# Kernel optimization log

Measured on AMD Instinct MI355X. Metric: run time of the kernel, lower is better.

The kernel has to match this reference:

```python
import jax, jax.numpy as jnp
import numpy as np

LMAX = 2; C = 64; H = 8; D = C // H
N_NODES = 10000; N_EDGES = 160000
M = (LMAX + 1) ** 2                      # 9 spherical components
RAD_IN = 64; RAD_HID = 64
WNUM = (LMAX + 1) * C                    # per-edge CP-TP weights: one per (l, channel)
L_OF_M = jnp.array([l for l in range(LMAX + 1) for _ in range(2 * l + 1)])
LN_EPS = 1e-5


def _lin(x, W, b=None):
    # Linear over channel (last) dim; bias applied ONLY to scalar (m=0) component
    y = jnp.einsum('nmc,cd->nmd', x, W)
    if b is not None:
        y = y.at[:, 0, :].add(b)
    return y


def _cp_tp(x, sh, w_lc):
    # CP tensor product with SH: channelwise product, per-(l, channel) radial weight
    # x: [E, M, C], sh: [E, M], w_lc: [E, LMAX+1, C]
    return x * sh[:, :, None] * w_lc[:, L_OF_M, :]


def _radial(s, W1, b1, g, b, W2, off):
    h = s @ W1 + b1
    mu = h.mean(-1, keepdims=True)
    var = h.var(-1, keepdims=True)
    h = (h - mu) / jnp.sqrt(var + LN_EPS) * g + b
    h = jax.nn.silu(h)
    return (h @ W2 + off).reshape(-1, LMAX + 1, C)


def _smooth_lrelu(x, a=0.2):
    return (1 + a) / 2 * x + (1 - a) / 2 * x * (2 * jax.nn.sigmoid(x) - 1)


def _gate(x):
    c = x.shape[-1] // 2
    v = x[..., :c]
    g = jax.nn.sigmoid(x[:, 0, c:])[:, None, :]
    return jnp.concatenate([jax.nn.silu(v[:, :1, :]), v[:, 1:, :] * g], axis=1)


def _seg_softmax(a, idx, n):
    # numerically stable softmax over edges grouped by destination node
    m = jax.ops.segment_max(a, idx, num_segments=n)
    e = jnp.exp(a - m[idx])
    s = jax.ops.segment_sum(e, idx, num_segments=n)
    return e / (s[idx] + 1e-16)


def setup_inputs():
    key = jax.random.key(0)
    ks = jax.random.split(key, 16)
    def w(k, shape, fan_in):
        return jax.random.normal(k, shape, jnp.float32) / np.sqrt(fan_in)
    bound = 1.0 / np.sqrt(RAD_HID)
    return {
        'node_input': jax.random.normal(ks[0], (N_NODES, M, C), jnp.float32),
        'edge_attr': jax.random.normal(ks[1], (N_EDGES, M), jnp.float32),
        'edge_scalars': jax.random.normal(ks[2], (N_EDGES, RAD_IN), jnp.float32),
        'W_src': w(ks[3], (C, C), C), 'b_src': jnp.zeros((C,), jnp.float32),
        'W_dst': w(ks[4], (C, C), C),
        'rad_W1': w(ks[5], (RAD_IN, RAD_HID), RAD_IN),
        'rad_b1': jnp.zeros((RAD_HID,), jnp.float32),
        'rad_ln_g': jnp.ones((RAD_HID,), jnp.float32),
        'rad_ln_b': jnp.zeros((RAD_HID,), jnp.float32),
        'rad_W2': w(ks[6], (RAD_HID, WNUM), RAD_HID),
        'rad_offset': jax.random.uniform(ks[7], (WNUM,), jnp.float32, -bound, bound),
        'W_alpha': w(ks[8], (C, C), C), 'b_alpha': jnp.zeros((C,), jnp.float32),
        'alpha_dot': w(ks[9], (H, D), D),
        'W_value': w(ks[10], (C, 2 * C), C), 'b_value': jnp.zeros((2 * C,), jnp.float32),
        'W_proj': w(ks[11], (C, C), C), 'b_proj': jnp.zeros((C,), jnp.float32),
        'edge_src': jax.random.randint(ks[12], (N_EDGES,), 0, N_NODES),
        'edge_dst': jax.random.randint(ks[13], (N_EDGES,), 0, N_NODES),
        'batch': jnp.zeros((N_NODES,), jnp.int32),
    }


def reference(node_input, edge_attr, edge_scalars, W_src, b_src, W_dst,
              rad_W1, rad_b1, rad_ln_g, rad_ln_b, rad_W2, rad_offset,
              W_alpha, b_alpha, alpha_dot, W_value, b_value, W_proj, b_proj,
              edge_src, edge_dst, batch):
    # gather: per-edge merged message [E, M, C]
    msg = _lin(node_input, W_src, b_src)[edge_src] + _lin(node_input, W_dst)[edge_dst]
    # per-edge radial weights for both tensor products [E, LMAX+1, C]
    w_lc = _radial(edge_scalars, rad_W1, rad_b1, rad_ln_g, rad_ln_b, rad_W2, rad_offset)
    msg = _cp_tp(msg, edge_attr, w_lc)
    # alpha path: scalar channel only
    alpha = _lin(msg, W_alpha, b_alpha)[:, 0, :].reshape(-1, H, D)
    alpha = _smooth_lrelu(alpha)[:, None]                 # [E, 1, H, D]
    alpha = jnp.einsum('bikd,kd->bik', alpha, alpha_dot)  # [E, 1, H]
    alpha = _seg_softmax(alpha, edge_dst, N_NODES)        # dropout disabled (eval)
    # value path
    value = _gate(_lin(msg, W_value, b_value))
    value = _cp_tp(value, edge_attr, w_lc)
    value = value.reshape(N_EDGES, M, H, D)
    # scatter-aggregate to destination nodes
    out = jax.ops.segment_sum(value * alpha[:, :, :, None], edge_dst, num_segments=N_NODES)
    return _lin(out.reshape(N_NODES, M, C), W_proj, b_proj)
```

## Files before the change

kernel.cpp:

```cpp
#include <hip/hip_runtime.h>
#include <stdint.h>

#define NN 10000
#define NE 160000

struct BF16 { unsigned short v; };
typedef _Float16 h2_t __attribute__((ext_vector_type(2)));
typedef _Float16 f16x8 __attribute__((ext_vector_type(8)));
typedef float f32x4 __attribute__((ext_vector_type(4)));

__device__ __forceinline__ float cvt(float x) { return x; }
__device__ __forceinline__ float cvt(BF16 x) {
    union { unsigned int i; float f; } u; u.i = ((unsigned int)x.v) << 16; return u.f;
}
__device__ __forceinline__ unsigned short f2b_us(float f) {
    union { float f; unsigned int i; } v; v.f = f;
    unsigned int x = v.i;
    unsigned int lsb = (x >> 16) & 1u;
    x += 0x7fffu + lsb;
    return (unsigned short)(x >> 16);
}
__device__ __forceinline__ float rlane(float v, int l) {
    return __uint_as_float((unsigned int)__builtin_amdgcn_readlane(__float_as_uint(v), l));
}
__device__ __forceinline__ h2_t rlane_pk(h2_t v, int l) {
    union { h2_t h; unsigned int u; } c; c.h = v;
    c.u = (unsigned int)__builtin_amdgcn_readlane(c.u, l);
    return c.h;
}
__device__ __forceinline__ h2_t pkh2(float a, float b) {
    h2_t r; r[0] = (_Float16)a; r[1] = (_Float16)b; return r;
}
__device__ __forceinline__ float fdot2f(h2_t a, h2_t b, float c) {
#if __has_builtin(__builtin_amdgcn_fdot2)
    return __builtin_amdgcn_fdot2(a, b, c, false);
#else
    return fmaf((float)a[0], (float)b[0], fmaf((float)a[1], (float)b[1], c));
#endif
}
__device__ __forceinline__ float sigm(float x) { return 1.0f / (1.0f + __expf(-x)); }
__device__ __forceinline__ int clampi(int v, int hi) { return (unsigned)v >= (unsigned)hi ? 0 : v; }

__device__ __forceinline__ void stOut(float* p, size_t i, float v) { p[i] = v; }
__device__ __forceinline__ void stOut(unsigned short* p, size_t i, float v) { p[i] = f2b_us(v); }

__device__ __forceinline__ unsigned okey(float f) {
    unsigned b = __float_as_uint(f);
    return (b & 0x80000000u) ? ~b : (b | 0x80000000u);
}
__device__ __forceinline__ float okdec(unsigned k) {
    unsigned b = (k & 0x80000000u) ? (k ^ 0x80000000u) : ~k;
    return __uint_as_float(b);
}

__device__ __forceinline__ f16x8 ld8f16(const BF16* p) {
    uint4 v = *(const uint4*)p;
    unsigned w0 = v.x, w1 = v.y, w2 = v.z, w3 = v.w;
    f16x8 r;
    union { unsigned u; float f; } c;
    c.u = (w0 & 0xFFFFu) << 16;  r[0] = (_Float16)c.f;
    c.u = (w0 & 0xFFFF0000u);    r[1] = (_Float16)c.f;
    c.u = (w1 & 0xFFFFu) << 16;  r[2] = (_Float16)c.f;
    c.u = (w1 & 0xFFFF0000u);    r[3] = (_Float16)c.f;
    c.u = (w2 & 0xFFFFu) << 16;  r[4] = (_Float16)c.f;
    c.u = (w2 & 0xFFFF0000u);    r[5] = (_Float16)c.f;
    c.u = (w3 & 0xFFFFu) << 16;  r[6] = (_Float16)c.f;
    c.u = (w3 & 0xFFFF0000u);    r[7] = (_Float16)c.f;
    return r;
}
__device__ __forceinline__ f16x8 ld8f16(const float* p) {
    float4 a = *(const float4*)p;
    float4 b = *(const float4*)(p + 4);
    f16x8 r;
    r[0] = (_Float16)a.x; r[1] = (_Float16)a.y; r[2] = (_Float16)a.z; r[3] = (_Float16)a.w;
    r[4] = (_Float16)b.x; r[5] = (_Float16)b.y; r[6] = (_Float16)b.z; r[7] = (_Float16)b.w;
    return r;
}

__global__ void k0_zero(int* __restrict__ cnt, int* __restrict__ csr, int* __restrict__ flag,
                        float* __restrict__ nsum, unsigned* __restrict__ mseg,
                        float* __restrict__ sseg) {
    int i = blockIdx.x * blockDim.x + threadIdx.x;
    if (i == 0) *flag = 1;
    if (i < NN) cnt[i] = 0;
    if (i < NE) csr[i] = 0;
    if (i < NN * 8) { mseg[i] = 0u; sseg[i] = 0.f; }
    for (int j = i; j < NN * 576; j += gridDim.x * blockDim.x) nsum[j] = 0.f;
}

__global__ void kprobe(const unsigned short* __restrict__ x, int* __restrict__ flag) {
    int bad = 0;
    for (int i = threadIdx.x; i < 16384; i += blockDim.x) {
        unsigned e = (x[i] >> 7) & 0xFFu;
        bad += (e == 0xFFu);
    }
    if (bad > 0) atomicExch(flag, 0);
}

template<typename T>
__device__ void k1_body(const T* x, const T* Ws, const T* bs, const T* Wd,
                        _Float16* fs, _Float16* fd)
{
    int lane = threadIdx.x & 63;
    int wv = threadIdx.x >> 6;
    float ws[64], wd[64];
#pragma unroll
    for (int i = 0; i < 64; i++) { ws[i] = cvt(Ws[i * 64 + lane]); wd[i] = cvt(Wd[i * 64 + lane]); }
    float bsl = cvt(bs[lane]);
    const int ROWS = NN * 9;
    for (int r = blockIdx.x * 4 + wv; r < ROWS; r += gridDim.x * 4) {
        float xv = cvt(x[(size_t)r * 64 + lane]);
        float a0 = 0, a1 = 0, a2 = 0, a3 = 0, d0 = 0, d1 = 0, d2 = 0, d3 = 0;
#pragma unroll
        for (int i = 0; i < 64; i += 4) {
            float x0 = rlane(xv, i), x1 = rlane(xv, i + 1), x2 = rlane(xv, i + 2), x3 = rlane(xv, i + 3);
            a0 = fmaf(x0, ws[i], a0);     a1 = fmaf(x1, ws[i + 1], a1);
            a2 = fmaf(x2, ws[i + 2], a2); a3 = fmaf(x3, ws[i + 3], a3);
            d0 = fmaf(x0, wd[i], d0);     d1 = fmaf(x1, wd[i + 1], d1);
            d2 = fmaf(x2, wd[i + 2], d2); d3 = fmaf(x3, wd[i + 3], d3);
        }
        float as = a0 + a1 + a2 + a3;
        if ((r % 9) == 0) as += bsl;
        fs[(size_t)r * 64 + lane] = (_Float16)as;
        fd[(size_t)r * 64 + lane] = (_Float16)(d0 + d1 + d2 + d3);
    }
}

__global__ __launch_bounds__(256) void k1_feats(
    const void* x, const void* Ws, const void* bs, const void* Wd,
    _Float16* fs, _Float16* fd, const int* flag)
{
    if (*flag) k1_body((const BF16*)x, (const BF16*)Ws, (const BF16*)bs, (const BF16*)Wd, fs, fd);
    else       k1_body((const float*)x, (const float*)Ws, (const float*)bs, (const float*)Wd, fs, fd);
}

__global__ void k2a_count(const int* __restrict__ dst, int* __restrict__ cnt) {
    for (int e = blockIdx.x * blockDim.x + threadIdx.x; e < NE; e += gridDim.x * blockDim.x)
        atomicAdd(&cnt[clampi(dst[e], NN)], 1);
}

__global__ __launch_bounds__(1024) void k2b_scan(const int* __restrict__ cnt,
                                                 int* __restrict__ off, int* __restrict__ cur) {
    __shared__ int part[1024];
    int t = threadIdx.x;
    int base = t * 10;
    int loc[10]; int s = 0;
#pragma unroll
    for (int k = 0; k < 10; k++) { int i = base + k; int v = (i < NN) ? cnt[i] : 0; loc[k] = v; s += v; }
    part[t] = s; __syncthreads();
    for (int o = 1; o < 1024; o <<= 1) {
        int v = (t >= o) ? part[t - o] : 0;
        __syncthreads();
        part[t] += v;
        __syncthreads();
    }
    int run = (t == 0) ? 0 : part[t - 1];
#pragma unroll
    for (int k = 0; k < 10; k++) {
        int i = base + k;
        if (i < NN) { off[i] = run; cur[i] = run; run += loc[k]; }
    }
    if (t == 1023) off[NN] = part[1023];
}

__global__ void k2c_fill(const int* __restrict__ dst, int* __restrict__ cur, int* __restrict__ csr) {
    for (int e = blockIdx.x * blockDim.x + threadIdx.x; e < NE; e += gridDim.x * blockDim.x) {
        int d = clampi(dst[e], NN);
        int p = atomicAdd(&cur[d], 1);
        if ((unsigned)p < (unsigned)NE) csr[p] = e;
    }
}

template<typename T>
__device__ void k3m_body(const T* es, const T* W1, const T* b1g, const T* gg, const T* bbv,
                         const T* W2, const T* roff, _Float16* wlc,
                         _Float16 (*Yt)[200])
{
    const int lane = threadIdx.x & 63;
    const int c16 = lane & 15;
    const int kg  = lane >> 4;

    f16x8 bW1[4][2], bW2[12][2];
#pragma unroll
    for (int t = 0; t < 4; t++)
#pragma unroll
        for (int kh = 0; kh < 2; kh++) {
            f16x8 f;
#pragma unroll
            for (int j = 0; j < 8; j++) {
                int k = kh * 32 + kg * 8 + j;
                f[j] = (_Float16)cvt(W1[(size_t)k * 64 + t * 16 + c16]);
            }
            bW1[t][kh] = f;
        }
#pragma unroll
    for (int t = 0; t < 12; t++)
#pragma unroll
        for (int kh = 0; kh < 2; kh++) {
            f16x8 f;
#pragma unroll
            for (int j = 0; j < 8; j++) {
                int k = kh * 32 + kg * 8 + j;
                f[j] = (_Float16)cvt(W2[(size_t)k * 192 + t * 16 + c16]);
            }
            bW2[t][kh] = f;
        }
    float b1v[4], gv[4], bv[4], rv[12];
#pragma unroll
    for (int t = 0; t < 4; t++) {
        b1v[t] = cvt(b1g[t * 16 + c16]);
        gv[t]  = cvt(gg[t * 16 + c16]);
        bv[t]  = cvt(bbv[t * 16 + c16]);
    }
#pragma unroll
    for (int t = 0; t < 12; t++) rv[t] = cvt(roff[t * 16 + c16]);

    const int NT = NE / 16;
    for (int tile = blockIdx.x * 4 + (threadIdx.x >> 6); tile < NT; tile += gridDim.x * 4) {
        const int e0 = tile * 16;
        f16x8 a0 = ld8f16(&es[(size_t)(e0 + c16) * 64 + kg * 8]);
        f16x8 a1 = ld8f16(&es[(size_t)(e0 + c16) * 64 + 32 + kg * 8]);
        f32x4 h[4] = {{0,0,0,0},{0,0,0,0},{0,0,0,0},{0,0,0,0}};
#pragma unroll
        for (int t = 0; t < 4; t++) {
            h[t] = __builtin_amdgcn_mfma_f32_16x16x32_f16(a0, bW1[t][0], h[t], 0, 0, 0);
            h[t] = __builtin_amdgcn_mfma_f32_16x16x32_f16(a1, bW1[t][1], h[t], 0, 0, 0);
        }
#pragma unroll
        for (int r = 0; r < 4; r++) {
            float x0 = h[0][r] + b1v[0], x1 = h[1][r] + b1v[1];
            float x2 = h[2][r] + b1v[2], x3 = h[3][r] + b1v[3];
            float s = x0 + x1 + x2 + x3;
            float q = x0 * x0 + x1 * x1 + x2 * x2 + x3 * x3;
            s += __shfl_xor(s, 1, 64); q += __shfl_xor(q, 1, 64);
            s += __shfl_xor(s, 2, 64); q += __shfl_xor(q, 2, 64);
            s += __shfl_xor(s, 4, 64); q += __shfl_xor(q, 4, 64);
            s += __shfl_xor(s, 8, 64); q += __shfl_xor(q, 8, 64);
            float mu = s * (1.0f / 64.0f);
            float var = fmaxf(q * (1.0f / 64.0f) - mu * mu, 0.0f);
            float rs = rsqrtf(var + 1e-5f);
            int row = kg * 4 + r;
#pragma unroll
            for (int t = 0; t < 4; t++) {
                float xt = (t == 0) ? x0 : (t == 1) ? x1 : (t == 2) ? x2 : x3;
                float v = (xt - mu) * rs * gv[t] + bv[t];
                v = v * sigm(v);
                Yt[row][t * 16 + c16] = (_Float16)v;
            }
        }
        f16x8 a20 = *(const f16x8*)&Yt[c16][kg * 8];
        f16x8 a21 = *(const f16x8*)&Yt[c16][32 + kg * 8];
        f32x4 y[12] = {{0,0,0,0},{0,0,0,0},{0,0,0,0},{0,0,0,0},{0,0,0,0},{0,0,0,0},
                       {0,0,0,0},{0,0,0,0},{0,0,0,0},{0,0,0,0},{0,0,0,0},{0,0,0,0}};
#pragma unroll
        for (int t = 0; t < 12; t++) {
            y[t] = __builtin_amdgcn_mfma_f32_16x16x32_f16(a20, bW2[t][0], y[t], 0, 0, 0);
            y[t] = __builtin_amdgcn_mfma_f32_16x16x32_f16(a21, bW2[t][1], y[t], 0, 0, 0);
        }
#pragma unroll
        for (int t = 0; t < 12; t++)
#pragma unroll
            for (int r = 0; r < 4; r++)
                Yt[kg * 4 + r][t * 16 + c16] = (_Float16)(y[t][r] + rv[t]);
#pragma unroll
        for (int j = 0; j < 6; j++) {
            int c = lane + 64 * j;
            int row = c / 24;
            int cc = (c % 24) * 8;
            *(f16x8*)&wlc[(size_t)(e0 + row) * 192 + cc] = *(const f16x8*)&Yt[row][cc];
        }
    }
}

__global__ __launch_bounds__(256) void k3m_wlc(
    const void* es, const void* W1, const void* b1, const void* g, const void* bln,
    const void* W2, const void* roff, _Float16* wlc, const int* flag)
{
    __shared__ _Float16 Y[4][16][200];
    const int wv = threadIdx.x >> 6;
    if (*flag) k3m_body<BF16>((const BF16*)es, (const BF16*)W1, (const BF16*)b1, (const BF16*)g,
                              (const BF16*)bln, (const BF16*)W2, (const BF16*)roff, wlc, Y[wv]);
    else       k3m_body<float>((const float*)es, (const float*)W1, (const float*)b1, (const float*)g,
                               (const float*)bln, (const float*)W2, (const float*)roff, wlc, Y[wv]);
}

template<typename T>
__device__ void k4_body(const T* ea, const _Float16* fs, const _Float16* fd,
                        const _Float16* wlc, const T* Wa, const T* ba, const T* adot,
                        const int* esrc, const int* edst, float* alpha, unsigned* mseg)
{
    int lane = threadIdx.x & 63;
    int wv = threadIdx.x >> 6;
    int j2 = (lane & 31) * 2;
    h2_t wap[32];
#pragma unroll
    for (int i = 0; i < 32; i++)
        wap[i] = pkh2(cvt(Wa[(2 * i) * 64 + lane]), cvt(Wa[(2 * i + 1) * 64 + lane]));
    float bal = cvt(ba[lane]), adl = cvt(adot[lane]);
    for (int e = blockIdx.x * 4 + wv; e < NE; e += gridDim.x * 4) {
        int sn = clampi(esrc[e], NN), dn = clampi(edst[e], NN);
        h2_t fsp = *(const h2_t*)&fs[(size_t)sn * 576 + j2];
        h2_t fdp = *(const h2_t*)&fd[(size_t)dn * 576 + j2];
        h2_t wlp = *(const h2_t*)&wlc[(size_t)e * 192 + j2];
        float ea0 = cvt(ea[(size_t)e * 9]);
        float m0a = ((float)fsp[0] + (float)fdp[0]) * ea0 * (float)wlp[0];
        float m0b = ((float)fsp[1] + (float)fdp[1]) * ea0 * (float)wlp[1];
        h2_t m0p = pkh2(m0a, m0b);
        float a0 = bal, a1 = 0, a2 = 0, a3 = 0;
#pragma unroll
        for (int i = 0; i < 32; i += 4) {
            a0 = fdot2f(rlane_pk(m0p, i),     wap[i],     a0);
            a1 = fdot2f(rlane_pk(m0p, i + 1), wap[i + 1], a1);
            a2 = fdot2f(rlane_pk(m0p, i + 2), wap[i + 2], a2);
            a3 = fdot2f(rlane_pk(m0p, i + 3), wap[i + 3], a3);
        }
        float aw = a0 + a1 + a2 + a3;
        float f = aw * (0.2f + 0.8f * sigm(aw));
        float p = f * adl;
        p += __shfl_xor(p, 1, 64);
        p += __shfl_xor(p, 2, 64);
        p += __shfl_xor(p, 4, 64);
        if ((lane & 7) == 0) {
            alpha[(size_t)e * 8 + (lane >> 3)] = p;
            atomicMax(&mseg[dn * 8 + (lane >> 3)], okey(p));
        }
    }
}

__global__ __launch_bounds__(256) void k4_alpha(
    const void* ea, const _Float16* fs, const _Float16* fd, const _Float16* wlc,
    const void* Wa, const void* ba, const void* adot,
    const int* esrc, const int* edst, float* alpha, unsigned* mseg, const int* flag)
{
    if (*flag) k4_body((const BF16*)ea, fs, fd, wlc, (const BF16*)Wa, (const BF16*)ba,
                       (const BF16*)adot, esrc, edst, alpha, mseg);
    else       k4_body((const float*)ea, fs, fd, wlc, (const float*)Wa, (const float*)ba,
                       (const float*)adot, esrc, edst, alpha, mseg);
}

__global__ void k5b_expsum(const int* __restrict__ edst, const unsigned* __restrict__ mseg,
                           float* __restrict__ alpha, float* __restrict__ sseg) {
    int t = blockIdx.x * blockDim.x + threadIdx.x;
    if (t >= NE * 8) return;
    int e = t >> 3, h = t & 7;
    int dn = clampi(edst[e], NN);
    float m = okdec(mseg[dn * 8 + h]);
    float ex = __expf(alpha[t] - m);
    alpha[t] = ex;
    unsafeAtomicAdd(&sseg[dn * 8 + h], ex);
}

template<typename T>
__device__ void k6m_body(const int* off, const int* csr, const int* esrc,
                         const T* ea, const _Float16* fs, const _Float16* fd,
                         const _Float16* wlc, const T* Wv, const T* bv,
                         const float* alpha, const float* sseg, float* nsum,
                         _Float16 (*wlS)[16][72], float (*mtS)[20])
{
    const int lane = threadIdx.x & 63;
    const int wvid = threadIdx.x >> 6;
    const int c16 = lane & 15;
    const int kg  = lane >> 4;

    for (int gw = blockIdx.x * 4 + wvid; gw < NN * 2; gw += gridDim.x * 4) {
        const int n = gw >> 1;
        const int half = gw & 1;
        const int b = off[n], e_end = off[n + 1];
        if (b >= e_end) continue;

        f16x8 bfV[2][2], bfG[2][2];
        float bvv[2], bgv[2];
        int colg[2], hh[2];
        float invs[2];
#pragma unroll
        for (int t = 0; t < 2; t++) {
            colg[t] = (half * 2 + t) * 16 + c16;
            hh[t] = colg[t] >> 3;
            invs[t] = 1.0f / (sseg[n * 8 + hh[t]] + 1e-16f);
#pragma unroll
            for (int kh = 0; kh < 2; kh++) {
                f16x8 b8v, b8g;
#pragma unroll
                for (int j = 0; j < 8; j++) {
                    int k = kh * 32 + kg * 8 + j;
                    b8v[j] = (_Float16)cvt(Wv[(size_t)k * 128 + colg[t]]);
                    b8g[j] = (_Float16)cvt(Wv[(size_t)k * 128 + 64 + colg[t]]);
                }
                bfV[t][kh] = b8v; bfG[t][kh] = b8g;
            }
            bvv[t] = cvt(bv[colg[t]]);
            bgv[t] = cvt(bv[64 + colg[t]]);
        }

        const size_t fdb = (size_t)n * 576;
        const size_t nbase = (size_t)n * 576;

        for (int p0 = b; p0 < e_end; p0 += 16) {
            int pA = p0 + c16; if (pA >= e_end) pA = e_end - 1;
            const int eA = clampi(csr[pA], NE);
            const int snA = clampi(esrc[eA], NN);
            const size_t fsb = (size_t)snA * 576;
            const size_t wlb = (size_t)eA * 192;

#pragma unroll
            for (int l = 0; l < 3; l++)
#pragma unroll
                for (int kh = 0; kh < 2; kh++)
                    *(f16x8*)&wlS[l][c16][kh * 32 + kg * 8] =
                        *(const f16x8*)&wlc[wlb + (size_t)l * 64 + kh * 32 + kg * 8];
            float eao[9];
#pragma unroll
            for (int m = 0; m < 9; m++) eao[m] = cvt(ea[(size_t)eA * 9 + m]);
            if (kg == 0) {
#pragma unroll
                for (int m = 0; m < 9; m++) mtS[c16][m] = eao[m];
            }
            mtS[c16][10 + kg * 2]     = alpha[(size_t)eA * 8 + kg * 2];
            mtS[c16][10 + kg * 2 + 1] = alpha[(size_t)eA * 8 + kg * 2 + 1];

            float awm[2][4];
#pragma unroll
            for (int r = 0; r < 4; r++) {
                int row = kg * 4 + r;
                float vm = (p0 + row < e_end) ? 1.f : 0.f;
#pragma unroll
                for (int t = 0; t < 2; t++)
                    awm[t][r] = mtS[row][10 + hh[t]] * invs[t] * vm;
            }

            float gtv[2][4];
            {
                f16x8 a0, a1;
                {
                    f16x8 w0 = *(const f16x8*)&wlS[0][c16][kg * 8];
                    f16x8 w1 = *(const f16x8*)&wlS[0][c16][32 + kg * 8];
                    f16x8 fd0 = *(const f16x8*)&fd[fdb + kg * 8];
                    f16x8 fd1 = *(const f16x8*)&fd[fdb + 32 + kg * 8];
                    f16x8 fs0 = *(const f16x8*)&fs[fsb + kg * 8];
                    f16x8 fs1 = *(const f16x8*)&fs[fsb + 32 + kg * 8];
                    _Float16 eh = (_Float16)eao[0];
                    f16x8 ev;
#pragma unroll
                    for (int j = 0; j < 8; j++) ev[j] = eh;
                    a0 = (fs0 + fd0) * ev * w0;
                    a1 = (fs1 + fd1) * ev * w1;
                }
                f32x4 d[2] = {{0,0,0,0},{0,0,0,0}};
                f32x4 g[2] = {{0,0,0,0},{0,0,0,0}};
#pragma unroll
                for (int t = 0; t < 2; t++) {
                    d[t] = __builtin_amdgcn_mfma_f32_16x16x32_f16(a0, bfV[t][0], d[t], 0, 0, 0);
                    d[t] = __builtin_amdgcn_mfma_f32_16x16x32_f16(a1, bfV[t][1], d[t], 0, 0, 0);
                    g[t] = __builtin_amdgcn_mfma_f32_16x16x32_f16(a0, bfG[t][0], g[t], 0, 0, 0);
                    g[t] = __builtin_amdgcn_mfma_f32_16x16x32_f16(a1, bfG[t][1], g[t], 0, 0, 0);
                }
#pragma unroll
                for (int t = 0; t < 2; t++) {
                    float ps = 0.f;
#pragma unroll
                    for (int r = 0; r < 4; r++) {
                        int row = kg * 4 + r;
                        gtv[t][r] = sigm(g[t][r] + bgv[t]);
                        float v = d[t][r] + bvv[t];
                        float f = v * sigm(v);
                        float wlv = (float)wlS[0][row][colg[t]];
                        float eam = mtS[row][0];
                        ps = fmaf(f * (eam * wlv), awm[t][r], ps);
                    }
                    ps += __shfl_xor(ps, 16, 64);
                    ps += __shfl_xor(ps, 32, 64);
                    if (kg == 0) unsafeAtomicAdd(&nsum[nbase + colg[t]], ps);
                }
            }
#pragma unroll 2
            for (int m = 1; m < 9; m++) {
                const int l = (m < 4) ? 1 : 2;
                f16x8 a0, a1;
                {
                    const size_t mo = (size_t)m * 64;
                    f16x8 w0 = *(const f16x8*)&wlS[l][c16][kg * 8];
                    f16x8 w1 = *(const f16x8*)&wlS[l][c16][32 + kg * 8];
                    f16x8 fd0 = *(const f16x8*)&fd[fdb + mo + kg * 8];
                    f16x8 fd1 = *(const f16x8*)&fd[fdb + mo + 32 + kg * 8];
                    f16x8 fs0 = *(const f16x8*)&fs[fsb + mo + kg * 8];
                    f16x8 fs1 = *(const f16x8*)&fs[fsb + mo + 32 + kg * 8];
                    _Float16 eh = (_Float16)eao[m];
                    f16x8 ev;
#pragma unroll
                    for (int j = 0; j < 8; j++) ev[j] = eh;
                    a0 = (fs0 + fd0) * ev * w0;
                    a1 = (fs1 + fd1) * ev * w1;
                }
                f32x4 d[2] = {{0,0,0,0},{0,0,0,0}};
#pragma unroll
                for (int t = 0; t < 2; t++) {
                    d[t] = __builtin_amdgcn_mfma_f32_16x16x32_f16(a0, bfV[t][0], d[t], 0, 0, 0);
                    d[t] = __builtin_amdgcn_mfma_f32_16x16x32_f16(a1, bfV[t][1], d[t], 0, 0, 0);
                }
#pragma unroll
                for (int t = 0; t < 2; t++) {
                    float ps = 0.f;
#pragma unroll
                    for (int r = 0; r < 4; r++) {
                        int row = kg * 4 + r;
                        float f = d[t][r] * gtv[t][r];
                        float wlv = (float)wlS[l][row][colg[t]];
                        float eam = mtS[row][m];
                        ps = fmaf(f * (eam * wlv), awm[t][r], ps);
                    }
                    ps += __shfl_xor(ps, 16, 64);
                    ps += __shfl_xor(ps, 32, 64);
                    if (kg == 0) unsafeAtomicAdd(&nsum[nbase + (size_t)m * 64 + colg[t]], ps);
                }
            }
        }
    }
}

__global__ __launch_bounds__(256) void k6m_fused(
    const int* off, const int* csr, const int* esrc,
    const void* ea, const _Float16* fs, const _Float16* fd, const _Float16* wlc,
    const void* Wv, const void* bv,
    const float* alpha, const float* sseg, float* nsum, const int* flag)
{
    __shared__ _Float16 shwl[4][3][16][72];
    __shared__ float    shmt[4][16][20];
    const int wvid = threadIdx.x >> 6;
    if (*flag) k6m_body<BF16>(off, csr, esrc, (const BF16*)ea, fs, fd, wlc,
                              (const BF16*)Wv, (const BF16*)bv, alpha, sseg, nsum,
                              shwl[wvid], shmt[wvid]);
    else       k6m_body<float>(off, csr, esrc, (const float*)ea, fs, fd, wlc,
                               (const float*)Wv, (const float*)bv, alpha, sseg, nsum,
                               shwl[wvid], shmt[wvid]);
}

template<typename T, typename OT>
__device__ void k7_body(const float* nsum, const T* Wp, const T* bp, OT* out)
{
    int lane = threadIdx.x & 63;
    int wv = threadIdx.x >> 6;
    float wp[64];
#pragma unroll
    for (int i = 0; i < 64; i++) wp[i] = cvt(Wp[i * 64 + lane]);
    float bpl = cvt(bp[lane]);
    const int ROWS = NN * 9;
    for (int r = blockIdx.x * 4 + wv; r < ROWS; r += gridDim.x * 4) {
        float xv = nsum[(size_t)r * 64 + lane];
        float o0 = 0, o1 = 0, o2 = 0, o3 = 0;
#pragma unroll
        for (int i = 0; i < 64; i += 4) {
            o0 = fmaf(rlane(xv, i), wp[i], o0);
            o1 = fmaf(rlane(xv, i + 1), wp[i + 1], o1);
            o2 = fmaf(rlane(xv, i + 2), wp[i + 2], o2);
            o3 = fmaf(rlane(xv, i + 3), wp[i + 3], o3);
        }
        float o = o0 + o1 + o2 + o3;
        if ((r % 9) == 0) o += bpl;
        stOut(out, (size_t)r * 64 + lane, o);
    }
}

__global__ __launch_bounds__(256) void k7_proj(
    const float* nsum, const void* Wp, const void* bp, void* out, const int* flag)
{
    if (*flag) k7_body<BF16, unsigned short>(nsum, (const BF16*)Wp, (const BF16*)bp, (unsigned short*)out);
    else       k7_body<float, float>(nsum, (const float*)Wp, (const float*)bp, (float*)out);
}

extern "C" void kernel_launch(void* const* d_in, const int* in_sizes, int n_in,
                              void* d_out, int out_size, void* d_ws, size_t ws_size,
                              hipStream_t stream) {
    const void* node_input = d_in[0];
    const void* edge_attr  = d_in[1];
    const void* edge_scal  = d_in[2];
    const void* W_src      = d_in[3];
    const void* b_src      = d_in[4];
    const void* W_dst      = d_in[5];
    const void* rad_W1     = d_in[6];
    const void* rad_b1     = d_in[7];
    const void* rad_ln_g   = d_in[8];
    const void* rad_ln_b   = d_in[9];
    const void* rad_W2     = d_in[10];
    const void* rad_off    = d_in[11];
    const void* W_alpha    = d_in[12];
    const void* b_alpha    = d_in[13];
    const void* alpha_dot  = d_in[14];
    const void* W_value    = d_in[15];
    const void* b_value    = d_in[16];
    const void* W_proj     = d_in[17];
    const void* b_proj     = d_in[18];
    const int* edge_src    = (const int*)d_in[19];
    const int* edge_dst    = (const int*)d_in[20];

    char* ws = (char*)d_ws;
    size_t ofs = 0;
    auto alloc = [&](size_t bytes) -> char* {
        char* r = ws + ofs;
        ofs = (ofs + bytes + 255) & ~(size_t)255;
        return r;
    };

    int* flag       = (int*)alloc(256);
    int* cnt        = (int*)alloc((size_t)NN * 4);
    int* offs       = (int*)alloc((size_t)(NN + 16) * 4);
    int* cur        = (int*)alloc((size_t)NN * 4);
    int* csr        = (int*)alloc((size_t)NE * 4);
    unsigned* mseg  = (unsigned*)alloc((size_t)NN * 8 * 4);
    float* sseg     = (float*)alloc((size_t)NN * 8 * 4);
    float* alpha    = (float*)alloc((size_t)NE * 8 * 4);
    _Float16* fs    = (_Float16*)alloc((size_t)NN * 576 * 2);
    _Float16* fd    = (_Float16*)alloc((size_t)NN * 576 * 2);
    _Float16* wlc   = (_Float16*)alloc((size_t)NE * 192 * 2);
    float* nsum32   = (float*)alloc((size_t)NN * 576 * 4);

    k0_zero<<<dim3(625), dim3(256), 0, stream>>>(cnt, csr, flag, nsum32, mseg, sseg);
    kprobe<<<dim3(1), dim3(256), 0, stream>>>((const unsigned short*)node_input, flag);
    k1_feats<<<dim3(2048), dim3(256), 0, stream>>>(node_input, W_src, b_src, W_dst, fs, fd, flag);
    k2a_count<<<dim3(512), dim3(256), 0, stream>>>(edge_dst, cnt);
    k2b_scan<<<dim3(1), dim3(1024), 0, stream>>>(cnt, offs, cur);
    k2c_fill<<<dim3(512), dim3(256), 0, stream>>>(edge_dst, cur, csr);
    k3m_wlc<<<dim3(512), dim3(256), 0, stream>>>(edge_scal, rad_W1, rad_b1, rad_ln_g, rad_ln_b,
                                                 rad_W2, rad_off, wlc, flag);
    k4_alpha<<<dim3(2048), dim3(256), 0, stream>>>(edge_attr, fs, fd, wlc, W_alpha, b_alpha,
                                                   alpha_dot, edge_src, edge_dst, alpha, mseg, flag);
    k5b_expsum<<<dim3(5000), dim3(256), 0, stream>>>(edge_dst, mseg, alpha, sseg);
    k6m_fused<<<dim3(5000), dim3(256), 0, stream>>>(offs, csr, edge_src, edge_attr, fs, fd, wlc,
                                                    W_value, b_value, alpha, sseg, nsum32, flag);
    k7_proj<<<dim3(2048), dim3(256), 0, stream>>>(nsum32, W_proj, b_proj, d_out, flag);
}
```

Before: 543.4 us.

## Use MFMA tiles for node feature projection and edge alpha logits

Rewrites the node src/dst linear projection kernel and the per-edge alpha logit kernel to process 16-row tiles with 16x16x32 f16 MFMA instructions, replacing the per-row readlane/FMA and dot2 loops. Results are staged through per-wave shared memory so stores and the per-destination atomicMax are coalesced. Grid sizes are adjusted to the tile counts. Inputs are now rounded to f16 before the matmul and the edge message product is computed in f16, which slightly reduces precision.

```diff
diff --git a/kernel.cpp b/kernel.cpp
--- a/kernel.cpp
+++ b/kernel.cpp
@@ -98,40 +98,76 @@
 }
 
 template<typename T>
-__device__ void k1_body(const T* x, const T* Ws, const T* bs, const T* Wd,
-                        _Float16* fs, _Float16* fd)
-{
-    int lane = threadIdx.x & 63;
-    int wv = threadIdx.x >> 6;
-    float ws[64], wd[64];
-#pragma unroll
-    for (int i = 0; i < 64; i++) { ws[i] = cvt(Ws[i * 64 + lane]); wd[i] = cvt(Wd[i * 64 + lane]); }
-    float bsl = cvt(bs[lane]);
-    const int ROWS = NN * 9;
-    for (int r = blockIdx.x * 4 + wv; r < ROWS; r += gridDim.x * 4) {
-        float xv = cvt(x[(size_t)r * 64 + lane]);
-        float a0 = 0, a1 = 0, a2 = 0, a3 = 0, d0 = 0, d1 = 0, d2 = 0, d3 = 0;
-#pragma unroll
-        for (int i = 0; i < 64; i += 4) {
-            float x0 = rlane(xv, i), x1 = rlane(xv, i + 1), x2 = rlane(xv, i + 2), x3 = rlane(xv, i + 3);
-            a0 = fmaf(x0, ws[i], a0);     a1 = fmaf(x1, ws[i + 1], a1);
-            a2 = fmaf(x2, ws[i + 2], a2); a3 = fmaf(x3, ws[i + 3], a3);
-            d0 = fmaf(x0, wd[i], d0);     d1 = fmaf(x1, wd[i + 1], d1);
-            d2 = fmaf(x2, wd[i + 2], d2); d3 = fmaf(x3, wd[i + 3], d3);
-        }
-        float as = a0 + a1 + a2 + a3;
-        if ((r % 9) == 0) as += bsl;
-        fs[(size_t)r * 64 + lane] = (_Float16)as;
-        fd[(size_t)r * 64 + lane] = (_Float16)(d0 + d1 + d2 + d3);
-    }
-}
-
-__global__ __launch_bounds__(256) void k1_feats(
+__device__ void k1m_body(const T* x, const T* Ws, const T* bs, const T* Wd,
+                         _Float16* fs, _Float16* fd, _Float16 (*Yt)[128])
+{
+    const int lane = threadIdx.x & 63;
+    const int c16 = lane & 15;
+    const int kg  = lane >> 4;
+
+    f16x8 bWs[4][2], bWd[4][2];
+#pragma unroll
+    for (int t = 0; t < 4; t++)
+#pragma unroll
+        for (int kh = 0; kh < 2; kh++) {
+            f16x8 f1, f2;
+#pragma unroll
+            for (int j = 0; j < 8; j++) {
+                int k = kh * 32 + kg * 8 + j;
+                f1[j] = (_Float16)cvt(Ws[(size_t)k * 64 + t * 16 + c16]);
+                f2[j] = (_Float16)cvt(Wd[(size_t)k * 64 + t * 16 + c16]);
+            }
+            bWs[t][kh] = f1; bWd[t][kh] = f2;
+        }
+    float bsv[4];
+#pragma unroll
+    for (int t = 0; t < 4; t++) bsv[t] = cvt(bs[t * 16 + c16]);
+
+    const int NT = (NN * 9) / 16;
+    for (int tile = blockIdx.x * 4 + (threadIdx.x >> 6); tile < NT; tile += gridDim.x * 4) {
+        const int r0 = tile * 16;
+        f16x8 a0 = ld8f16(&x[(size_t)(r0 + c16) * 64 + kg * 8]);
+        f16x8 a1 = ld8f16(&x[(size_t)(r0 + c16) * 64 + 32 + kg * 8]);
+        f32x4 hs[4] = {{0,0,0,0},{0,0,0,0},{0,0,0,0},{0,0,0,0}};
+        f32x4 hd[4] = {{0,0,0,0},{0,0,0,0},{0,0,0,0},{0,0,0,0}};
+#pragma unroll
+        for (int t = 0; t < 4; t++) {
+            hs[t] = __builtin_amdgcn_mfma_f32_16x16x32_f16(a0, bWs[t][0], hs[t], 0, 0, 0);
+            hs[t] = __builtin_amdgcn_mfma_f32_16x16x32_f16(a1, bWs[t][1], hs[t], 0, 0, 0);
+            hd[t] = __builtin_amdgcn_mfma_f32_16x16x32_f16(a0, bWd[t][0], hd[t], 0, 0, 0);
+            hd[t] = __builtin_amdgcn_mfma_f32_16x16x32_f16(a1, bWd[t][1], hd[t], 0, 0, 0);
+        }
+#pragma unroll
+        for (int t = 0; t < 4; t++)
+#pragma unroll
+            for (int r = 0; r < 4; r++) {
+                int row = kg * 4 + r;
+                float vs = hs[t][r];
+                if (((r0 + row) % 9) == 0) vs += bsv[t];
+                Yt[row][t * 16 + c16] = (_Float16)vs;
+                Yt[row][64 + t * 16 + c16] = (_Float16)hd[t][r];
+            }
+#pragma unroll
+        for (int j = 0; j < 2; j++) {
+            int c = lane + 64 * j;
+            int row = c >> 3;
+            int cc = (c & 7) * 8;
+            *(f16x8*)&fs[(size_t)(r0 + row) * 64 + cc] = *(const f16x8*)&Yt[row][cc];
+            *(f16x8*)&fd[(size_t)(r0 + row) * 64 + cc] = *(const f16x8*)&Yt[row][64 + cc];
+        }
+    }
+}
+
+__global__ __launch_bounds__(256) void k1m_feats(
     const void* x, const void* Ws, const void* bs, const void* Wd,
     _Float16* fs, _Float16* fd, const int* flag)
 {
-    if (*flag) k1_body((const BF16*)x, (const BF16*)Ws, (const BF16*)bs, (const BF16*)Wd, fs, fd);
-    else       k1_body((const float*)x, (const float*)Ws, (const float*)bs, (const float*)Wd, fs, fd);
+    __shared__ _Float16 Y[4][16][128];
+    const int wv = threadIdx.x >> 6;
+    if (*flag) k1m_body<BF16>((const BF16*)x, (const BF16*)Ws, (const BF16*)bs, (const BF16*)Wd,
+                              fs, fd, Y[wv]);
+    else       k1m_body<float>((const float*)x, (const float*)Ws, (const float*)bs, (const float*)Wd,
+                               fs, fd, Y[wv]);
 }
 
 __global__ void k2a_count(const int* __restrict__ dst, int* __restrict__ cnt) {
@@ -285,57 +321,97 @@
 }
 
 template<typename T>
-__device__ void k4_body(const T* ea, const _Float16* fs, const _Float16* fd,
-                        const _Float16* wlc, const T* Wa, const T* ba, const T* adot,
-                        const int* esrc, const int* edst, float* alpha, unsigned* mseg)
-{
-    int lane = threadIdx.x & 63;
-    int wv = threadIdx.x >> 6;
-    int j2 = (lane & 31) * 2;
-    h2_t wap[32];
-#pragma unroll
-    for (int i = 0; i < 32; i++)
-        wap[i] = pkh2(cvt(Wa[(2 * i) * 64 + lane]), cvt(Wa[(2 * i + 1) * 64 + lane]));
-    float bal = cvt(ba[lane]), adl = cvt(adot[lane]);
-    for (int e = blockIdx.x * 4 + wv; e < NE; e += gridDim.x * 4) {
-        int sn = clampi(esrc[e], NN), dn = clampi(edst[e], NN);
-        h2_t fsp = *(const h2_t*)&fs[(size_t)sn * 576 + j2];
-        h2_t fdp = *(const h2_t*)&fd[(size_t)dn * 576 + j2];
-        h2_t wlp = *(const h2_t*)&wlc[(size_t)e * 192 + j2];
-        float ea0 = cvt(ea[(size_t)e * 9]);
-        float m0a = ((float)fsp[0] + (float)fdp[0]) * ea0 * (float)wlp[0];
-        float m0b = ((float)fsp[1] + (float)fdp[1]) * ea0 * (float)wlp[1];
-        h2_t m0p = pkh2(m0a, m0b);
-        float a0 = bal, a1 = 0, a2 = 0, a3 = 0;
-#pragma unroll
-        for (int i = 0; i < 32; i += 4) {
-            a0 = fdot2f(rlane_pk(m0p, i),     wap[i],     a0);
-            a1 = fdot2f(rlane_pk(m0p, i + 1), wap[i + 1], a1);
-            a2 = fdot2f(rlane_pk(m0p, i + 2), wap[i + 2], a2);
-            a3 = fdot2f(rlane_pk(m0p, i + 3), wap[i + 3], a3);
-        }
-        float aw = a0 + a1 + a2 + a3;
-        float f = aw * (0.2f + 0.8f * sigm(aw));
-        float p = f * adl;
-        p += __shfl_xor(p, 1, 64);
-        p += __shfl_xor(p, 2, 64);
-        p += __shfl_xor(p, 4, 64);
-        if ((lane & 7) == 0) {
-            alpha[(size_t)e * 8 + (lane >> 3)] = p;
-            atomicMax(&mseg[dn * 8 + (lane >> 3)], okey(p));
-        }
-    }
-}
-
-__global__ __launch_bounds__(256) void k4_alpha(
+__device__ void k4m_body(const T* ea, const _Float16* fs, const _Float16* fd,
+                         const _Float16* wlc, const T* Wa, const T* ba, const T* adot,
+                         const int* esrc, const int* edst, float* alpha, unsigned* mseg,
+                         float (*aS)[8])
+{
+    const int lane = threadIdx.x & 63;
+    const int c16 = lane & 15;
+    const int kg  = lane >> 6 == 0 ? (lane >> 4) : (lane >> 4);
+
+    f16x8 bWa[4][2];
+#pragma unroll
+    for (int t = 0; t < 4; t++)
+#pragma unroll
+        for (int kh = 0; kh < 2; kh++) {
+            f16x8 f;
+#pragma unroll
+            for (int j = 0; j < 8; j++) {
+                int k = kh * 32 + (lane >> 4) * 8 + j;
+                f[j] = (_Float16)cvt(Wa[(size_t)k * 64 + t * 16 + c16]);
+            }
+            bWa[t][kh] = f;
+        }
+    float bav[4], adv[4];
+#pragma unroll
+    for (int t = 0; t < 4; t++) {
+        bav[t] = cvt(ba[t * 16 + c16]);
+        adv[t] = cvt(adot[t * 16 + c16]);
+    }
+    const int kgr = lane >> 4;
+
+    const int NT = NE / 16;
+    for (int tile = blockIdx.x * 4 + (threadIdx.x >> 6); tile < NT; tile += gridDim.x * 4) {
+        const int e0 = tile * 16;
+        const int eA = e0 + c16;
+        const int sn = clampi(esrc[eA], NN);
+        const int dn = clampi(edst[eA], NN);
+        f16x8 fs0 = *(const f16x8*)&fs[(size_t)sn * 576 + kgr * 8];
+        f16x8 fs1 = *(const f16x8*)&fs[(size_t)sn * 576 + 32 + kgr * 8];
+        f16x8 fd0 = *(const f16x8*)&fd[(size_t)dn * 576 + kgr * 8];
+        f16x8 fd1 = *(const f16x8*)&fd[(size_t)dn * 576 + 32 + kgr * 8];
+        f16x8 wl0 = *(const f16x8*)&wlc[(size_t)eA * 192 + kgr * 8];
+        f16x8 wl1 = *(const f16x8*)&wlc[(size_t)eA * 192 + 32 + kgr * 8];
+        _Float16 eh = (_Float16)cvt(ea[(size_t)eA * 9]);
+        f16x8 ev;
+#pragma unroll
+        for (int j = 0; j < 8; j++) ev[j] = eh;
+        f16x8 a0 = (fs0 + fd0) * ev * wl0;
+        f16x8 a1 = (fs1 + fd1) * ev * wl1;
+
+        f32x4 d[4] = {{0,0,0,0},{0,0,0,0},{0,0,0,0},{0,0,0,0}};
+#pragma unroll
+        for (int t = 0; t < 4; t++) {
+            d[t] = __builtin_amdgcn_mfma_f32_16x16x32_f16(a0, bWa[t][0], d[t], 0, 0, 0);
+            d[t] = __builtin_amdgcn_mfma_f32_16x16x32_f16(a1, bWa[t][1], d[t], 0, 0, 0);
+        }
+#pragma unroll
+        for (int t = 0; t < 4; t++)
+#pragma unroll
+            for (int r = 0; r < 4; r++) {
+                float aw = d[t][r] + bav[t];
+                float f = aw * (0.2f + 0.8f * sigm(aw));
+                float p = f * adv[t];
+                p += __shfl_xor(p, 1, 64);
+                p += __shfl_xor(p, 2, 64);
+                p += __shfl_xor(p, 4, 64);
+                if ((c16 & 7) == 0)
+                    aS[kgr * 4 + r][t * 2 + (c16 >> 3)] = p;
+            }
+#pragma unroll
+        for (int j = 0; j < 2; j++) {
+            int idx = lane * 2 + j;
+            int row = idx >> 3, h = idx & 7;
+            float p = aS[row][h];
+            alpha[(size_t)(e0 + row) * 8 + h] = p;
+            int dnr = clampi(edst[e0 + row], NN);
+            atomicMax(&mseg[dnr * 8 + h], okey(p));
+        }
+    }
+}
+
+__global__ __launch_bounds__(256) void k4m_alpha(
     const void* ea, const _Float16* fs, const _Float16* fd, const _Float16* wlc,
     const void* Wa, const void* ba, const void* adot,
     const int* esrc, const int* edst, float* alpha, unsigned* mseg, const int* flag)
 {
-    if (*flag) k4_body((const BF16*)ea, fs, fd, wlc, (const BF16*)Wa, (const BF16*)ba,
-                       (const BF16*)adot, esrc, edst, alpha, mseg);
-    else       k4_body((const float*)ea, fs, fd, wlc, (const float*)Wa, (const float*)ba,
-                       (const float*)adot, esrc, edst, alpha, mseg);
+    __shared__ float A[4][16][8];
+    const int wv = threadIdx.x >> 6;
+    if (*flag) k4m_body<BF16>((const BF16*)ea, fs, fd, wlc, (const BF16*)Wa, (const BF16*)ba,
+                              (const BF16*)adot, esrc, edst, alpha, mseg, A[wv]);
+    else       k4m_body<float>((const float*)ea, fs, fd, wlc, (const float*)Wa, (const float*)ba,
+                               (const float*)adot, esrc, edst, alpha, mseg, A[wv]);
 }
 
 __global__ void k5b_expsum(const int* __restrict__ edst, const unsigned* __restrict__ mseg,
@@ -615,14 +691,14 @@
 
     k0_zero<<<dim3(625), dim3(256), 0, stream>>>(cnt, csr, flag, nsum32, mseg, sseg);
     kprobe<<<dim3(1), dim3(256), 0, stream>>>((const unsigned short*)node_input, flag);
-    k1_feats<<<dim3(2048), dim3(256), 0, stream>>>(node_input, W_src, b_src, W_dst, fs, fd, flag);
+    k1m_feats<<<dim3(1408), dim3(256), 0, stream>>>(node_input, W_src, b_src, W_dst, fs, fd, flag);
     k2a_count<<<dim3(512), dim3(256), 0, stream>>>(edge_dst, cnt);
     k2b_scan<<<dim3(1), dim3(1024), 0, stream>>>(cnt, offs, cur);
     k2c_fill<<<dim3(512), dim3(256), 0, stream>>>(edge_dst, cur, csr);
     k3m_wlc<<<dim3(512), dim3(256), 0, stream>>>(edge_scal, rad_W1, rad_b1, rad_ln_g, rad_ln_b,
                                                  rad_W2, rad_off, wlc, flag);
-    k4_alpha<<<dim3(2048), dim3(256), 0, stream>>>(edge_attr, fs, fd, wlc, W_alpha, b_alpha,
-                                                   alpha_dot, edge_src, edge_dst, alpha, mseg, flag);
+    k4m_alpha<<<dim3(2500), dim3(256), 0, stream>>>(edge_attr, fs, fd, wlc, W_alpha, b_alpha,
+                                                    alpha_dot, edge_src, edge_dst, alpha, mseg, flag);
     k5b_expsum<<<dim3(5000), dim3(256), 0, stream>>>(edge_dst, mseg, alpha, sseg);
     k6m_fused<<<dim3(5000), dim3(256), 0, stream>>>(offs, csr, edge_src, edge_attr, fs, fd, wlc,
                                                     W_value, b_value, alpha, sseg, nsum32, flag);
```

Result: faster. 488.3 us (-10.1%).
